# Kernel tuning notes

Measured on AMD Instinct MI355X. Metric: run time of the kernel, lower is better.

Reference implementation:

```python
import jax, jax.numpy as jnp
import numpy as np

H = W = 64      # input_resolution
WS = 8          # window_size
SS = 4          # shift_size
DIM = 96
HEADS = 4
HEAD_DIM = DIM // HEADS
SCALE = HEAD_DIM ** -0.5
N = WS * WS     # tokens per window
EPS = 1e-5


def _rel_pos_index():
    # static (N, N) int index into the (2*WS-1)^2 bias table
    coords = np.stack(np.meshgrid(np.arange(WS), np.arange(WS), indexing='ij'))  # (2, WS, WS)
    cf = coords.reshape(2, -1)                       # (2, N)
    rel = (cf[:, :, None] - cf[:, None, :]).transpose(1, 2, 0)  # (N, N, 2)
    rel[:, :, 0] += WS - 1
    rel[:, :, 1] += WS - 1
    rel[:, :, 0] *= 2 * WS - 1
    return rel.sum(-1)                               # (N, N)


def _attn_mask():
    # static (nW, N, N) 0/-100 mask for shifted windows
    img = np.zeros((H, W))
    cnt = 0
    sl = (slice(0, -WS), slice(-WS, -SS), slice(-SS, None))
    for hs in sl:
        for ws_ in sl:
            img[hs, ws_] = cnt
            cnt += 1
    mw = img.reshape(H // WS, WS, W // WS, WS).transpose(0, 2, 1, 3).reshape(-1, N)
    diff = mw[:, None, :] - mw[:, :, None]
    return np.where(diff != 0, -100.0, 0.0).astype(np.float32)


_RPI = jnp.asarray(_rel_pos_index())
_MASK = jnp.asarray(_attn_mask())  # (nW, N, N)


def _layernorm(x, g, b):
    mu = jnp.mean(x, axis=-1, keepdims=True)
    var = jnp.mean(jnp.square(x - mu), axis=-1, keepdims=True)
    return (x - mu) * jax.lax.rsqrt(var + EPS) * g + b


def setup_inputs() -> dict:
    key = jax.random.key(0)
    ks = jax.random.split(key, 8)
    s = 0.02
    return {
        'x': jax.random.normal(ks[0], (64, H * W, DIM), jnp.float32),
        'norm1_g': jnp.ones((DIM,), jnp.float32),
        'norm1_b': jnp.zeros((DIM,), jnp.float32),
        'qkv_w': jax.random.normal(ks[1], (3 * DIM, DIM), jnp.float32) * s,
        'qkv_b': jnp.zeros((3 * DIM,), jnp.float32),
        'rel_bias_table': jax.random.normal(ks[2], ((2 * WS - 1) ** 2, HEADS), jnp.float32) * s,
        'proj_w': jax.random.normal(ks[3], (DIM, DIM), jnp.float32) * s,
        'proj_b': jnp.zeros((DIM,), jnp.float32),
        'norm2_g': jnp.ones((DIM,), jnp.float32),
        'norm2_b': jnp.zeros((DIM,), jnp.float32),
        'fc1_w': jax.random.normal(ks[4], (4 * DIM, DIM), jnp.float32) * s,
        'fc1_b': jnp.zeros((4 * DIM,), jnp.float32),
        'fc2_w': jax.random.normal(ks[5], (DIM, 4 * DIM), jnp.float32) * s,
        'fc2_b': jnp.zeros((DIM,), jnp.float32),
    }


def reference(x, norm1_g, norm1_b, qkv_w, qkv_b, rel_bias_table, proj_w, proj_b,
              norm2_g, norm2_b, fc1_w, fc1_b, fc2_w, fc2_b):
    B, L, C = x.shape
    nW = (H // WS) * (W // WS)
    shortcut = x

    h = _layernorm(x, norm1_g, norm1_b).reshape(B, H, W, C)
    h = jnp.roll(h, (-SS, -SS), axis=(1, 2))
    # window partition -> (B*nW, N, C)
    h = h.reshape(B, H // WS, WS, W // WS, WS, C).transpose(0, 1, 3, 2, 4, 5)
    h = h.reshape(B * nW, N, C)

    qkv = h @ qkv_w.T + qkv_b                                   # (B_, N, 3C)
    qkv = qkv.reshape(B * nW, N, 3, HEADS, HEAD_DIM).transpose(2, 0, 3, 1, 4)
    q, k, v = qkv[0] * SCALE, qkv[1], qkv[2]                    # (B_, heads, N, hd)

    attn = jnp.einsum('whnd,whmd->whnm', q, k)                  # (B_, heads, N, N)
    bias = rel_bias_table[_RPI.reshape(-1)].reshape(N, N, HEADS).transpose(2, 0, 1)
    attn = attn + bias[None]
    attn = attn.reshape(B, nW, HEADS, N, N) + _MASK[None, :, None]
    attn = jax.nn.softmax(attn.reshape(B * nW, HEADS, N, N), axis=-1)

    out = jnp.einsum('whnm,whmd->whnd', attn, v)                # (B_, heads, N, hd)
    out = out.transpose(0, 2, 1, 3).reshape(B * nW, N, C)
    out = out @ proj_w.T + proj_b

    # window reverse + un-shift
    out = out.reshape(B, H // WS, W // WS, WS, WS, C).transpose(0, 1, 3, 2, 4, 5)
    out = out.reshape(B, H, W, C)
    out = jnp.roll(out, (SS, SS), axis=(1, 2)).reshape(B, L, C)

    x = shortcut + out
    h2 = _layernorm(x, norm2_g, norm2_b)
    h2 = jax.nn.gelu(h2 @ fc1_w.T + fc1_b, approximate=False)
    h2 = h2 @ fc2_w.T + fc2_b
    return x + h2
```

## Files before the change

### kernel.cpp

```cpp
#include <hip/hip_runtime.h>
#include <hip/hip_fp16.h>
#include <math.h>

typedef _Float16 half_t;
typedef _Float16 half8 __attribute__((ext_vector_type(8)));
typedef float f32x4 __attribute__((ext_vector_type(4)));

#define MFMA(a, b, c) __builtin_amdgcn_mfma_f32_16x16x32_f16((a), (b), (c), 0, 0, 0)

static constexpr float kScale = 0.2041241452319315f;
static constexpr int QSTR = 200;
static constexpr int VTS  = 72;
static constexpr int XNS  = 104;

__global__ __launch_bounds__(256) void k_convert(const float* __restrict__ qkv_w,
                                                 const float* __restrict__ proj_w,
                                                 const float* __restrict__ fc1_w,
                                                 const float* __restrict__ fc2_w,
                                                 const float* __restrict__ tbl,
                                                 half_t* __restrict__ wbuf,
                                                 float* __restrict__ biasT) {
  int i = blockIdx.x * 256 + threadIdx.x;
  if (i < 27648)        wbuf[i] = (half_t)qkv_w[i];
  else if (i < 36864)   wbuf[i] = (half_t)proj_w[i - 27648];
  else if (i < 73728)   wbuf[i] = (half_t)fc1_w[i - 36864];
  else if (i < 110592)  wbuf[i] = (half_t)fc2_w[i - 73728];
  else if (biasT != nullptr) {
    int j = i - 110592;
    int h = j >> 12, rem = j & 4095;
    int ii = rem >> 6, jj = rem & 63;
    int ih = ii >> 3, iw = ii & 7, jh = jj >> 3, jw = jj & 7;
    biasT[j] = tbl[((ih - jh + 7) * 15 + (iw - jw + 7)) * 4 + h];
  }
}

__global__ __launch_bounds__(256, 4) void k_swin(
    const float* __restrict__ x,
    const float* __restrict__ n1g, const float* __restrict__ n1b,
    const half_t* __restrict__ qkvw, const float* __restrict__ qkv_b,
    const float* __restrict__ tbl_g, const float* __restrict__ biasT,
    const half_t* __restrict__ projw, const float* __restrict__ proj_b,
    const float* __restrict__ n2g, const float* __restrict__ n2b,
    const half_t* __restrict__ fc1w, const float* __restrict__ fc1b,
    const half_t* __restrict__ fc2w, const float* __restrict__ fc2b,
    float* __restrict__ out) {
  __shared__ __attribute__((aligned(16))) unsigned char smem[40640];
  half_t* qbuf = (half_t*)smem;
  half_t* vbuf = (half_t*)(smem + 25600);

  int tid = threadIdx.x;
  int wave = tid >> 6, lane = tid & 63;
  int l15 = lane & 15, quad = lane >> 4;
  int blk = blockIdx.x;
  int bb = blk >> 6, wh = (blk >> 3) & 7, ww = blk & 7;

  half8 af[3];
  {
    int tok = wave * 16 + l15;
    int sr = (wh * 8 + (tok >> 3) + 4) & 63;
    int sc = (ww * 8 + (tok & 7) + 4) & 63;
    const float* rp = x + ((size_t)bb * 4096 + sr * 64 + sc) * 96;
    float v[24];
    float s1 = 0.f, s2 = 0.f;
#pragma unroll
    for (int kt = 0; kt < 3; ++kt) {
      float4 a = *(const float4*)(rp + kt * 32 + quad * 8);
      float4 b = *(const float4*)(rp + kt * 32 + quad * 8 + 4);
      v[kt*8+0]=a.x; v[kt*8+1]=a.y; v[kt*8+2]=a.z; v[kt*8+3]=a.w;
      v[kt*8+4]=b.x; v[kt*8+5]=b.y; v[kt*8+6]=b.z; v[kt*8+7]=b.w;
    }
#pragma unroll
    for (int c = 0; c < 24; ++c) { s1 += v[c]; s2 += v[c] * v[c]; }
    s1 += __shfl_xor(s1, 16); s1 += __shfl_xor(s1, 32);
    s2 += __shfl_xor(s2, 16); s2 += __shfl_xor(s2, 32);
    float mu = s1 * (1.f / 96.f);
    float inv = rsqrtf(fmaxf(s2 * (1.f / 96.f) - mu * mu, 0.f) + 1e-5f);
#pragma unroll
    for (int kt = 0; kt < 3; ++kt) {
      int c0 = kt * 32 + quad * 8;
      float4 g0 = *(const float4*)(n1g + c0);
      float4 g1 = *(const float4*)(n1g + c0 + 4);
      float4 b0 = *(const float4*)(n1b + c0);
      float4 b1 = *(const float4*)(n1b + c0 + 4);
      float gg[8] = {g0.x,g0.y,g0.z,g0.w,g1.x,g1.y,g1.z,g1.w};
      float bv[8] = {b0.x,b0.y,b0.z,b0.w,b1.x,b1.y,b1.z,b1.w};
      half8 hh;
#pragma unroll
      for (int j = 0; j < 8; ++j)
        hh[j] = (half_t)((v[kt*8+j] - mu) * inv * gg[j] + bv[j]);
      af[kt] = hh;
    }
  }

  {
#pragma unroll
    for (int t = 0; t < 18; ++t) {
      int n0 = t * 16 + l15;
      const half_t* wp = qkvw + (size_t)n0 * 96 + quad * 8;
      half8 b0 = *(const half8*)(wp);
      half8 b1 = *(const half8*)(wp + 32);
      half8 b2 = *(const half8*)(wp + 64);
      f32x4 acc = {0, 0, 0, 0};
      acc = MFMA(af[0], b0, acc);
      acc = MFMA(af[1], b1, acc);
      acc = MFMA(af[2], b2, acc);
      float bias = qkv_b[n0];
      if (t < 12) {
        float sc_ = (t < 6) ? kScale : 1.f;
#pragma unroll
        for (int r = 0; r < 4; ++r)
          qbuf[(wave * 16 + quad * 4 + r) * QSTR + n0] = (half_t)((acc[r] + bias) * sc_);
      } else {
        int vc = n0 - 192;
        int hd = vc / 24, c = vc - hd * 24;
#pragma unroll
        for (int r = 0; r < 4; ++r)
          vbuf[hd * 24 * VTS + c * VTS + wave * 16 + quad * 4 + r] = (half_t)(acc[r] + bias);
      }
    }
  }
  __syncthreads();

  {
    int head = wave;
    const half8 z8 = {};
    half8 kb[4], vb[2][2];
#pragma unroll
    for (int nt = 0; nt < 4; ++nt) {
      half8 t = *(const half8*)(&qbuf[(nt * 16 + l15) * QSTR + 96 + head * 24 + quad * 8]);
      kb[nt] = (quad < 3) ? t : z8;
    }
#pragma unroll
    for (int nt = 0; nt < 2; ++nt)
#pragma unroll
      for (int kt = 0; kt < 2; ++kt)
        vb[nt][kt] = *(const half8*)(&vbuf[head * 24 * VTS + (nt * 16 + l15) * VTS + kt * 32 + quad * 8]);

    int rj[4], jh_[4], jw_[4];
#pragma unroll
    for (int nt = 0; nt < 4; ++nt) {
      int j = nt * 16 + l15;
      jh_[nt] = j >> 3; jw_[nt] = j & 7;
      int rr = wh * 8 + jh_[nt], cc = ww * 8 + jw_[nt];
      rj[nt] = ((rr < 56) ? 0 : ((rr < 60) ? 1 : 2)) * 3 + ((cc < 56) ? 0 : ((cc < 60) ? 1 : 2));
    }

    half_t* pb = vbuf + head * 24 * VTS;
    f32x4 oacc[4][2];

#pragma unroll
    for (int g2 = 0; g2 < 4; ++g2) {
      half8 qt = *(const half8*)(&qbuf[(g2 * 16 + l15) * QSTR + head * 24 + quad * 8]);
      half8 qa = (quad < 3) ? qt : z8;
      f32x4 sv[4];
#pragma unroll
      for (int nt = 0; nt < 4; ++nt) {
        f32x4 a = {0, 0, 0, 0};
        sv[nt] = MFMA(qa, kb[nt], a);
      }
      float pinv[4];
#pragma unroll
      for (int r = 0; r < 4; ++r) {
        int i = g2 * 16 + quad * 4 + r;
        int ih = i >> 3, iw = i & 7;
        int rr = wh * 8 + ih, cc = ww * 8 + iw;
        int ri = ((rr < 56) ? 0 : ((rr < 60) ? 1 : 2)) * 3 + ((cc < 56) ? 0 : ((cc < 60) ? 1 : 2));
        float bvv[4];
        if (biasT != nullptr) {
          const float* bp = biasT + (head << 12) + (i << 6) + l15;
#pragma unroll
          for (int nt = 0; nt < 4; ++nt) bvv[nt] = bp[nt * 16];
        } else {
#pragma unroll
          for (int nt = 0; nt < 4; ++nt)
            bvv[nt] = tbl_g[((ih - jh_[nt] + 7) * 15 + (iw - jw_[nt] + 7)) * 4 + head];
        }
#pragma unroll
        for (int nt = 0; nt < 4; ++nt) {
          float val = sv[nt][r] + bvv[nt];
          if (ri != rj[nt]) val -= 100.f;
          sv[nt][r] = val;
        }
        float mx = fmaxf(fmaxf(sv[0][r], sv[1][r]), fmaxf(sv[2][r], sv[3][r]));
        mx = fmaxf(mx, __shfl_xor(mx, 1));
        mx = fmaxf(mx, __shfl_xor(mx, 2));
        mx = fmaxf(mx, __shfl_xor(mx, 4));
        mx = fmaxf(mx, __shfl_xor(mx, 8));
        float sum = 0.f;
#pragma unroll
        for (int nt = 0; nt < 4; ++nt) {
          float e = __expf(sv[nt][r] - mx);
          sv[nt][r] = e;
          sum += e;
        }
        sum += __shfl_xor(sum, 1);
        sum += __shfl_xor(sum, 2);
        sum += __shfl_xor(sum, 4);
        sum += __shfl_xor(sum, 8);
        pinv[r] = __builtin_amdgcn_rcpf(sum);
      }
#pragma unroll
      for (int nt = 0; nt < 4; ++nt)
#pragma unroll
        for (int r = 0; r < 4; ++r)
          pb[(quad * 4 + r) * VTS + nt * 16 + l15] = (half_t)(sv[nt][r] * pinv[r]);
      __builtin_amdgcn_sched_barrier(0);
      half8 pa0 = *(const half8*)(&pb[l15 * VTS + quad * 8]);
      half8 pa1 = *(const half8*)(&pb[l15 * VTS + 32 + quad * 8]);
#pragma unroll
      for (int nt = 0; nt < 2; ++nt) {
        f32x4 a = {0, 0, 0, 0};
        a = MFMA(pa0, vb[nt][0], a);
        a = MFMA(pa1, vb[nt][1], a);
        oacc[g2][nt] = a;
      }
    }
#pragma unroll
    for (int g2 = 0; g2 < 4; ++g2)
#pragma unroll
      for (int nt = 0; nt < 2; ++nt) {
        int c = nt * 16 + l15;
        if (c < 24)
#pragma unroll
          for (int r = 0; r < 4; ++r)
            qbuf[(g2 * 16 + quad * 4 + r) * QSTR + head * 24 + c] = (half_t)oacc[g2][nt][r];
      }
  }
  __syncthreads();

  float rv[6][4];
  int foff[4];
  half8 a5[3];
  {
    half8 oa[3];
#pragma unroll
    for (int kt = 0; kt < 3; ++kt)
      oa[kt] = *(const half8*)(&qbuf[(wave * 16 + l15) * QSTR + kt * 32 + quad * 8]);
    f32x4 acc[6];
#pragma unroll
    for (int t = 0; t < 6; ++t) {
      int n0 = t * 16 + l15;
      const half_t* wp = projw + (size_t)n0 * 96 + quad * 8;
      half8 b0 = *(const half8*)(wp);
      half8 b1 = *(const half8*)(wp + 32);
      half8 b2 = *(const half8*)(wp + 64);
      f32x4 a = {0, 0, 0, 0};
      a = MFMA(oa[0], b0, a);
      a = MFMA(oa[1], b1, a);
      a = MFMA(oa[2], b2, a);
      acc[t] = a;
    }
    float xv[6][4];
#pragma unroll
    for (int r = 0; r < 4; ++r) {
      int tok = wave * 16 + quad * 4 + r;
      int sr = (wh * 8 + (tok >> 3) + 4) & 63;
      int sc = (ww * 8 + (tok & 7) + 4) & 63;
      foff[r] = (bb * 4096 + sr * 64 + sc) * 96 + l15;
      const float* xp = x + foff[r];
#pragma unroll
      for (int t = 0; t < 6; ++t) xv[t][r] = xp[t * 16];
    }
    float s1[4] = {0, 0, 0, 0}, s2[4] = {0, 0, 0, 0};
#pragma unroll
    for (int t = 0; t < 6; ++t) {
      float pbv = proj_b[t * 16 + l15];
#pragma unroll
      for (int r = 0; r < 4; ++r) {
        float vvv = xv[t][r] + acc[t][r] + pbv;
        rv[t][r] = vvv;
        s1[r] += vvv; s2[r] += vvv * vvv;
      }
    }
    float mu[4], nv[4];
#pragma unroll
    for (int r = 0; r < 4; ++r) {
      s1[r] += __shfl_xor(s1[r], 1); s1[r] += __shfl_xor(s1[r], 2);
      s1[r] += __shfl_xor(s1[r], 4); s1[r] += __shfl_xor(s1[r], 8);
      s2[r] += __shfl_xor(s2[r], 1); s2[r] += __shfl_xor(s2[r], 2);
      s2[r] += __shfl_xor(s2[r], 4); s2[r] += __shfl_xor(s2[r], 8);
      mu[r] = s1[r] * (1.f / 96.f);
      nv[r] = rsqrtf(fmaxf(s2[r] * (1.f / 96.f) - mu[r] * mu[r], 0.f) + 1e-5f);
    }
    half_t* xnb = vbuf;
#pragma unroll
    for (int t = 0; t < 6; ++t) {
      int n0 = t * 16 + l15;
      float gv = n2g[n0], bv = n2b[n0];
#pragma unroll
      for (int r = 0; r < 4; ++r)
        xnb[(wave * 16 + quad * 4 + r) * XNS + n0] =
            (half_t)((rv[t][r] - mu[r]) * nv[r] * gv + bv);
    }
    __builtin_amdgcn_sched_barrier(0);
#pragma unroll
    for (int kt = 0; kt < 3; ++kt)
      a5[kt] = *(const half8*)(&xnb[(wave * 16 + l15) * XNS + kt * 32 + quad * 8]);
  }

  f32x4 acc6[6];
#pragma unroll
  for (int t = 0; t < 6; ++t) acc6[t] = (f32x4){0, 0, 0, 0};
#pragma unroll 1
  for (int kb = 0; kb < 2; ++kb) {
#pragma unroll
    for (int th = 0; th < 12; ++th) {
      int n0 = (kb * 12 + th) * 16 + l15;
      const half_t* wp = fc1w + (size_t)n0 * 96 + quad * 8;
      half8 b0 = *(const half8*)(wp);
      half8 b1 = *(const half8*)(wp + 32);
      half8 b2 = *(const half8*)(wp + 64);
      f32x4 a = {0, 0, 0, 0};
      a = MFMA(a5[0], b0, a);
      a = MFMA(a5[1], b1, a);
      a = MFMA(a5[2], b2, a);
      float fb = fc1b[n0];
#pragma unroll
      for (int r = 0; r < 4; ++r) {
        float vvv = a[r] + fb;
        float u = vvv * (1.5957691216f + 0.1427096322f * vvv * vvv);
        float g = vvv * __builtin_amdgcn_rcpf(1.f + __expf(-u));
        qbuf[(wave * 16 + quad * 4 + r) * QSTR + th * 16 + l15] = (half_t)g;
      }
    }
    __builtin_amdgcn_sched_barrier(0);
#pragma unroll
    for (int kk = 0; kk < 6; ++kk) {
      half8 ha = *(const half8*)(&qbuf[(wave * 16 + l15) * QSTR + kk * 32 + quad * 8]);
#pragma unroll
      for (int t6 = 0; t6 < 6; ++t6) {
        half8 bf = *(const half8*)(fc2w + (size_t)(t6 * 16 + l15) * 384 + kb * 192 + kk * 32 + quad * 8);
        acc6[t6] = MFMA(ha, bf, acc6[t6]);
      }
    }
    __builtin_amdgcn_sched_barrier(0);
  }

#pragma unroll
  for (int t6 = 0; t6 < 6; ++t6) {
    float fb = fc2b[t6 * 16 + l15];
#pragma unroll
    for (int r = 0; r < 4; ++r)
      out[(size_t)foff[r] + t6 * 16] = rv[t6][r] + acc6[t6][r] + fb;
  }
}

extern "C" void kernel_launch(void* const* d_in, const int* in_sizes, int n_in,
                              void* d_out, int out_size, void* d_ws, size_t ws_size,
                              hipStream_t stream) {
  const float* x      = (const float*)d_in[0];
  const float* n1g    = (const float*)d_in[1];
  const float* n1b    = (const float*)d_in[2];
  const float* qkv_w  = (const float*)d_in[3];
  const float* qkv_b  = (const float*)d_in[4];
  const float* rtbl   = (const float*)d_in[5];
  const float* proj_w = (const float*)d_in[6];
  const float* proj_b = (const float*)d_in[7];
  const float* n2g    = (const float*)d_in[8];
  const float* n2b    = (const float*)d_in[9];
  const float* fc1_w  = (const float*)d_in[10];
  const float* fc1_b  = (const float*)d_in[11];
  const float* fc2_w  = (const float*)d_in[12];
  const float* fc2_b  = (const float*)d_in[13];
  float* out = (float*)d_out;

  if (ws_size < 221184) return;
  half_t* wbuf = (half_t*)d_ws;
  float* biasT = (ws_size >= 221184 + 65536) ? (float*)((char*)d_ws + 221184) : nullptr;

  k_convert<<<496, 256, 0, stream>>>(qkv_w, proj_w, fc1_w, fc2_w, rtbl, wbuf, biasT);
  k_swin<<<4096, 256, 0, stream>>>(x, n1g, n1b, wbuf, qkv_b, rtbl, biasT,
                                   wbuf + 27648, proj_b, n2g, n2b,
                                   wbuf + 36864, fc1_b, wbuf + 73728, fc2_b, out);
}
```

Before: 468.5 us.

## Split GEMM output columns across waves to share weight loads across all rows

```diff
diff --git a/kernel.cpp b/kernel.cpp
--- a/kernel.cpp
+++ b/kernel.cpp
@@ -9,9 +9,10 @@
 #define MFMA(a, b, c) __builtin_amdgcn_mfma_f32_16x16x32_f16((a), (b), (c), 0, 0, 0)
 
 static constexpr float kScale = 0.2041241452319315f;
+static constexpr int RS   = 104;
 static constexpr int QSTR = 200;
 static constexpr int VTS  = 72;
-static constexpr int XNS  = 104;
+static constexpr int H1S  = 392;
 
 __global__ __launch_bounds__(256) void k_convert(const float* __restrict__ qkv_w,
                                                  const float* __restrict__ proj_w,
@@ -34,7 +35,7 @@
   }
 }
 
-__global__ __launch_bounds__(256, 4) void k_swin(
+__global__ __launch_bounds__(256, 3) void k_swin(
     const float* __restrict__ x,
     const float* __restrict__ n1g, const float* __restrict__ n1b,
     const half_t* __restrict__ qkvw, const float* __restrict__ qkv_b,
@@ -44,9 +45,13 @@
     const half_t* __restrict__ fc1w, const float* __restrict__ fc1b,
     const half_t* __restrict__ fc2w, const float* __restrict__ fc2b,
     float* __restrict__ out) {
-  __shared__ __attribute__((aligned(16))) unsigned char smem[40640];
+  __shared__ __attribute__((aligned(16))) unsigned char smem[52736];
   half_t* qbuf = (half_t*)smem;
-  half_t* vbuf = (half_t*)(smem + 25600);
+  half_t* h1h  = (half_t*)smem;
+  half_t* vT   = (half_t*)(smem + 25600);
+  half_t* rbuf = (half_t*)(smem + 25600);
+  half_t* hn   = (half_t*)(smem + 39424);
+  half_t* xn   = (half_t*)(smem + 39424);
 
   int tid = threadIdx.x;
   int wave = tid >> 6, lane = tid & 63;
@@ -54,7 +59,6 @@
   int blk = blockIdx.x;
   int bb = blk >> 6, wh = (blk >> 3) & 7, ww = blk & 7;
 
-  half8 af[3];
   {
     int tok = wave * 16 + l15;
     int sr = (wh * 8 + (tok >> 3) + 4) & 63;
@@ -88,34 +92,47 @@
 #pragma unroll
       for (int j = 0; j < 8; ++j)
         hh[j] = (half_t)((v[kt*8+j] - mu) * inv * gg[j] + bv[j]);
-      af[kt] = hh;
-    }
-  }
+      *(half8*)(&hn[tok * RS + kt * 32 + quad * 8]) = hh;
+    }
+  }
+  __syncthreads();
 
   {
-#pragma unroll
-    for (int t = 0; t < 18; ++t) {
+    half8 af[4][3];
+#pragma unroll
+    for (int g = 0; g < 4; ++g)
+#pragma unroll
+      for (int kt = 0; kt < 3; ++kt)
+        af[g][kt] = *(const half8*)(&hn[(g * 16 + l15) * RS + kt * 32 + quad * 8]);
+    for (int t = wave; t < 18; t += 4) {
       int n0 = t * 16 + l15;
       const half_t* wp = qkvw + (size_t)n0 * 96 + quad * 8;
       half8 b0 = *(const half8*)(wp);
       half8 b1 = *(const half8*)(wp + 32);
       half8 b2 = *(const half8*)(wp + 64);
-      f32x4 acc = {0, 0, 0, 0};
-      acc = MFMA(af[0], b0, acc);
-      acc = MFMA(af[1], b1, acc);
-      acc = MFMA(af[2], b2, acc);
+      f32x4 acc[4] = {{0,0,0,0},{0,0,0,0},{0,0,0,0},{0,0,0,0}};
+#pragma unroll
+      for (int g = 0; g < 4; ++g) acc[g] = MFMA(af[g][0], b0, acc[g]);
+#pragma unroll
+      for (int g = 0; g < 4; ++g) acc[g] = MFMA(af[g][1], b1, acc[g]);
+#pragma unroll
+      for (int g = 0; g < 4; ++g) acc[g] = MFMA(af[g][2], b2, acc[g]);
       float bias = qkv_b[n0];
       if (t < 12) {
         float sc_ = (t < 6) ? kScale : 1.f;
 #pragma unroll
-        for (int r = 0; r < 4; ++r)
-          qbuf[(wave * 16 + quad * 4 + r) * QSTR + n0] = (half_t)((acc[r] + bias) * sc_);
+        for (int g = 0; g < 4; ++g)
+#pragma unroll
+          for (int r = 0; r < 4; ++r)
+            qbuf[(g * 16 + quad * 4 + r) * QSTR + n0] = (half_t)((acc[g][r] + bias) * sc_);
       } else {
         int vc = n0 - 192;
         int hd = vc / 24, c = vc - hd * 24;
 #pragma unroll
-        for (int r = 0; r < 4; ++r)
-          vbuf[hd * 24 * VTS + c * VTS + wave * 16 + quad * 4 + r] = (half_t)(acc[r] + bias);
+        for (int g = 0; g < 4; ++g)
+#pragma unroll
+          for (int r = 0; r < 4; ++r)
+            vT[hd * 24 * VTS + c * VTS + g * 16 + quad * 4 + r] = (half_t)(acc[g][r] + bias);
       }
     }
   }
@@ -134,7 +151,7 @@
     for (int nt = 0; nt < 2; ++nt)
 #pragma unroll
       for (int kt = 0; kt < 2; ++kt)
-        vb[nt][kt] = *(const half8*)(&vbuf[head * 24 * VTS + (nt * 16 + l15) * VTS + kt * 32 + quad * 8]);
+        vb[nt][kt] = *(const half8*)(&vT[head * 24 * VTS + (nt * 16 + l15) * VTS + kt * 32 + quad * 8]);
 
     int rj[4], jh_[4], jw_[4];
 #pragma unroll
@@ -145,7 +162,7 @@
       rj[nt] = ((rr < 56) ? 0 : ((rr < 60) ? 1 : 2)) * 3 + ((cc < 56) ? 0 : ((cc < 60) ? 1 : 2));
     }
 
-    half_t* pb = vbuf + head * 24 * VTS;
+    half_t* pb = vT + head * 24 * VTS;
     f32x4 oacc[4][2];
 
 #pragma unroll
@@ -228,9 +245,6 @@
   }
   __syncthreads();
 
-  float rv[6][4];
-  int foff[4];
-  half8 a5[3];
   {
     half8 oa[3];
 #pragma unroll
@@ -256,11 +270,11 @@
       int tok = wave * 16 + quad * 4 + r;
       int sr = (wh * 8 + (tok >> 3) + 4) & 63;
       int sc = (ww * 8 + (tok & 7) + 4) & 63;
-      foff[r] = (bb * 4096 + sr * 64 + sc) * 96 + l15;
-      const float* xp = x + foff[r];
+      const float* xp = x + ((size_t)bb * 4096 + sr * 64 + sc) * 96 + l15;
 #pragma unroll
       for (int t = 0; t < 6; ++t) xv[t][r] = xp[t * 16];
     }
+    float rv[6][4];
     float s1[4] = {0, 0, 0, 0}, s2[4] = {0, 0, 0, 0};
 #pragma unroll
     for (int t = 0; t < 6; ++t) {
@@ -282,66 +296,82 @@
       mu[r] = s1[r] * (1.f / 96.f);
       nv[r] = rsqrtf(fmaxf(s2[r] * (1.f / 96.f) - mu[r] * mu[r], 0.f) + 1e-5f);
     }
-    half_t* xnb = vbuf;
 #pragma unroll
     for (int t = 0; t < 6; ++t) {
       int n0 = t * 16 + l15;
       float gv = n2g[n0], bv = n2b[n0];
 #pragma unroll
-      for (int r = 0; r < 4; ++r)
-        xnb[(wave * 16 + quad * 4 + r) * XNS + n0] =
-            (half_t)((rv[t][r] - mu[r]) * nv[r] * gv + bv);
-    }
-    __builtin_amdgcn_sched_barrier(0);
-#pragma unroll
-    for (int kt = 0; kt < 3; ++kt)
-      a5[kt] = *(const half8*)(&xnb[(wave * 16 + l15) * XNS + kt * 32 + quad * 8]);
-  }
-
-  f32x4 acc6[6];
-#pragma unroll
-  for (int t = 0; t < 6; ++t) acc6[t] = (f32x4){0, 0, 0, 0};
-#pragma unroll 1
-  for (int kb = 0; kb < 2; ++kb) {
-#pragma unroll
-    for (int th = 0; th < 12; ++th) {
-      int n0 = (kb * 12 + th) * 16 + l15;
-      const half_t* wp = fc1w + (size_t)n0 * 96 + quad * 8;
-      half8 b0 = *(const half8*)(wp);
-      half8 b1 = *(const half8*)(wp + 32);
-      half8 b2 = *(const half8*)(wp + 64);
-      f32x4 a = {0, 0, 0, 0};
-      a = MFMA(a5[0], b0, a);
-      a = MFMA(a5[1], b1, a);
-      a = MFMA(a5[2], b2, a);
-      float fb = fc1b[n0];
-#pragma unroll
       for (int r = 0; r < 4; ++r) {
-        float vvv = a[r] + fb;
-        float u = vvv * (1.5957691216f + 0.1427096322f * vvv * vvv);
-        float g = vvv * __builtin_amdgcn_rcpf(1.f + __expf(-u));
-        qbuf[(wave * 16 + quad * 4 + r) * QSTR + th * 16 + l15] = (half_t)g;
-      }
-    }
-    __builtin_amdgcn_sched_barrier(0);
-#pragma unroll
-    for (int kk = 0; kk < 6; ++kk) {
-      half8 ha = *(const half8*)(&qbuf[(wave * 16 + l15) * QSTR + kk * 32 + quad * 8]);
-#pragma unroll
-      for (int t6 = 0; t6 < 6; ++t6) {
-        half8 bf = *(const half8*)(fc2w + (size_t)(t6 * 16 + l15) * 384 + kb * 192 + kk * 32 + quad * 8);
-        acc6[t6] = MFMA(ha, bf, acc6[t6]);
-      }
-    }
-    __builtin_amdgcn_sched_barrier(0);
-  }
-
-#pragma unroll
-  for (int t6 = 0; t6 < 6; ++t6) {
-    float fb = fc2b[t6 * 16 + l15];
-#pragma unroll
-    for (int r = 0; r < 4; ++r)
-      out[(size_t)foff[r] + t6 * 16] = rv[t6][r] + acc6[t6][r] + fb;
+        int row = wave * 16 + quad * 4 + r;
+        rbuf[row * RS + n0] = (half_t)rv[t][r];
+        xn[row * RS + n0] = (half_t)((rv[t][r] - mu[r]) * nv[r] * gv + bv);
+      }
+    }
+  }
+  __syncthreads();
+
+  for (int hb = 0; hb < 2; ++hb) {
+    {
+      half8 a5[2][3];
+#pragma unroll
+      for (int g2 = 0; g2 < 2; ++g2)
+#pragma unroll
+        for (int kt = 0; kt < 3; ++kt)
+          a5[g2][kt] = *(const half8*)(&xn[((hb * 2 + g2) * 16 + l15) * RS + kt * 32 + quad * 8]);
+      for (int t = wave; t < 24; t += 4) {
+        int n0 = t * 16 + l15;
+        const half_t* wp = fc1w + (size_t)n0 * 96 + quad * 8;
+        half8 b0 = *(const half8*)(wp);
+        half8 b1 = *(const half8*)(wp + 32);
+        half8 b2 = *(const half8*)(wp + 64);
+        f32x4 acc[2] = {{0,0,0,0},{0,0,0,0}};
+#pragma unroll
+        for (int g2 = 0; g2 < 2; ++g2) acc[g2] = MFMA(a5[g2][0], b0, acc[g2]);
+#pragma unroll
+        for (int g2 = 0; g2 < 2; ++g2) acc[g2] = MFMA(a5[g2][1], b1, acc[g2]);
+#pragma unroll
+        for (int g2 = 0; g2 < 2; ++g2) acc[g2] = MFMA(a5[g2][2], b2, acc[g2]);
+        float bias = fc1b[n0];
+#pragma unroll
+        for (int g2 = 0; g2 < 2; ++g2)
+#pragma unroll
+          for (int r = 0; r < 4; ++r) {
+            float vvv = acc[g2][r] + bias;
+            float u = vvv * (1.5957691216f + 0.1427096322f * vvv * vvv);
+            float g = vvv * __builtin_amdgcn_rcpf(1.f + __expf(-u));
+            h1h[(g2 * 16 + quad * 4 + r) * H1S + n0] = (half_t)g;
+          }
+      }
+    }
+    __syncthreads();
+    {
+      int rt = wave >> 1, chh = wave & 1;
+      half8 a2[12];
+#pragma unroll
+      for (int kt = 0; kt < 12; ++kt)
+        a2[kt] = *(const half8*)(&h1h[(rt * 16 + l15) * H1S + kt * 32 + quad * 8]);
+#pragma unroll
+      for (int i = 0; i < 3; ++i) {
+        int t = chh * 3 + i;
+        f32x4 acc = {0, 0, 0, 0};
+#pragma unroll
+        for (int kt = 0; kt < 12; ++kt) {
+          half8 bf = *(const half8*)(fc2w + (size_t)(t * 16 + l15) * 384 + kt * 32 + quad * 8);
+          acc = MFMA(a2[kt], bf, acc);
+        }
+        int col = t * 16 + l15;
+        float bias = fc2b[col];
+#pragma unroll
+        for (int r = 0; r < 4; ++r) {
+          int tok = hb * 32 + rt * 16 + quad * 4 + r;
+          int sr = (wh * 8 + (tok >> 3) + 4) & 63;
+          int sc = (ww * 8 + (tok & 7) + 4) & 63;
+          size_t fidx = ((size_t)bb * 4096 + sr * 64 + sc) * 96 + col;
+          out[fidx] = (float)rbuf[tok * RS + col] + acc[r] + bias;
+        }
+      }
+    }
+    __syncthreads();
   }
 }
 
```

After: 436.5 us. -6.8%, faster.
